# Kernel tuning notes

Measured on AMD Instinct MI355X. Metric: run time of the kernel, lower is better.

The kernel has to match this reference:

```python
import jax, jax.numpy as jnp
import numpy as np

N = 500000   # nodes per graph batch
E = 8000000  # edges per graph batch
B = 4096     # number of graphs
C = 2        # node feature dim
D = 2        # edge feature dim


def setup_inputs() -> dict:
    key = jax.random.key(0)
    ks = jax.random.split(key, 16)
    inp = {
        "x_a": jax.random.normal(ks[0], (N, C), jnp.float32),
        "edge_index_a": jax.random.randint(ks[1], (2, E), 0, N, jnp.int32),
        "edge_attr_a": jax.random.normal(ks[2], (E, D), jnp.float32),
        "batch_a": jnp.sort(jax.random.randint(ks[3], (N,), 0, B, jnp.int32)),
        "x_b": jax.random.normal(ks[4], (N, C), jnp.float32),
        "edge_index_b": jax.random.randint(ks[5], (2, E), 0, N, jnp.int32),
        "edge_attr_b": jax.random.normal(ks[6], (E, D), jnp.float32),
        "batch_b": jnp.sort(jax.random.randint(ks[7], (N,), 0, B, jnp.int32)),
        "targets": jax.random.normal(ks[8], (B,), jnp.float32),
        "num_graphs": B,
        # CGConv params: lin_f, lin_s each Linear(2*C+D=6 -> C)
        "Wf": jax.random.normal(ks[9], (2 * C + D, C), jnp.float32) * 0.4,
        "bf": jnp.zeros((C,), jnp.float32),
        "Ws": jax.random.normal(ks[10], (2 * C + D, C), jnp.float32) * 0.4,
        "bs": jnp.zeros((C,), jnp.float32),
        # l1: Linear(2 -> 3), l2: Linear(6 -> 1)
        "W1": jax.random.normal(ks[11], (C, 3), jnp.float32) * 0.5,
        "b1": jnp.zeros((3,), jnp.float32),
        "W2": jax.random.normal(ks[12], (6, 1), jnp.float32) * 0.4,
        "b2": jnp.zeros((1,), jnp.float32),
    }
    return inp


def cg_conv(x, edge_index, edge_attr, Wf, bf, Ws, bs):
    # PyG CGConv: out_i = x_i + sum_{j->i} sigmoid(lin_f(z)) * softplus(lin_s(z)),
    # z = [x_i, x_j, e_ij]; source_to_target flow => i = edge_index[1].
    src, dst = edge_index[0], edge_index[1]
    z = jnp.concatenate([x[dst], x[src], edge_attr], axis=1)  # [E, 6]
    m = jax.nn.sigmoid(z @ Wf + bf) * jax.nn.softplus(z @ Ws + bs)  # [E, C]
    agg = jax.ops.segment_sum(m, dst, num_segments=x.shape[0])
    return x + agg


def branch(x, edge_index, edge_attr, batch, num_graphs,
           Wf, bf, Ws, bs, W1, b1):
    h = cg_conv(x, edge_index, edge_attr, Wf, bf, Ws, bs)
    h = jax.nn.relu(h @ W1 + b1)  # [N, 3]
    sums = jax.ops.segment_sum(h, batch, num_segments=num_graphs)
    cnts = jax.ops.segment_sum(jnp.ones((h.shape[0],), h.dtype), batch,
                               num_segments=num_graphs)
    return sums / jnp.maximum(cnts, 1.0)[:, None]  # global_mean_pool [B, 3]


def reference(x_a, edge_index_a, edge_attr_a, batch_a,
              x_b, edge_index_b, edge_attr_b, batch_b,
              targets, num_graphs,
              Wf, bf, Ws, bs, W1, b1, W2, b2):
    out_1 = branch(x_a, edge_index_a, edge_attr_a, batch_a, num_graphs,
                   Wf, bf, Ws, bs, W1, b1)
    out_2 = branch(x_b, edge_index_b, edge_attr_b, batch_b, num_graphs,
                   Wf, bf, Ws, bs, W1, b1)
    out = jnp.concatenate([out_1, out_2], axis=1)  # [B, 6]
    out = jax.nn.relu(out @ W2 + b2)               # [B, 1]
    loss = jnp.mean((out[:, 0] - targets) ** 2)
    return out, loss
```

## Files before the change

kernel.cpp:

```cpp
#include <hip/hip_runtime.h>

#define N_NODES 500000
#define N_EDGES 8000000
#define N_GRAPHS 4096

#define NB 128
#define BIN_SHIFT 12
#define BIN_NODES 4096
#define NBINS 123
#define BIN_CAP 66560
#define T_EDGES 8192
#define P1_THREADS 512
#define EPT (T_EDGES / P1_THREADS)
#define P1_GRID ((N_EDGES + T_EDGES - 1) / T_EDGES)
#define K 4
#define P2_GRID (NBINS * K)
#define SLICE_F (BIN_NODES * 2)
#define FXS 131072.0f
#define FXI (1.0f / 131072.0f)
#define M_MAX 250.0f
#define OVF_CAP 8192

#define OFF_CURS_A   0
#define OFF_CURS_B   512
#define OFF_OVFC_A   1024
#define OFF_OVFC_B   1280
#define ZERO_SMALL   1536
#define OFF_STARTS_A 4096
#define OFF_STARTS_B 20736
#define OFF_MEAN_A   37376
#define OFF_MEAN_B   86528
#define OFF_OVF_A    135680
#define OFF_OVF_B    266752
#define OFF_SCRATCH  397824
#define OFF_BINS     16519680
#define WS_NEED      82014720ull

__global__ __launch_bounds__(512, 4) void p1_kernel(
    const float* __restrict__ x, const int* __restrict__ ei,
    const float* __restrict__ ea,
    const float* __restrict__ Wf, const float* __restrict__ bfv,
    const float* __restrict__ Ws, const float* __restrict__ bsv,
    unsigned long long* __restrict__ bins, unsigned int* __restrict__ cursors,
    unsigned int* __restrict__ ovf_cnt, float4* __restrict__ ovf)
{
    __shared__ unsigned long long sorted[T_EDGES];
    __shared__ unsigned int whist[8][NB];
    __shared__ unsigned int base[NB];
    __shared__ unsigned int cur[NB];
    __shared__ unsigned int gbase[NB];
    __shared__ unsigned int ntot_s;

    int t = threadIdx.x;
    int wave = t >> 6;
    int ebase = blockIdx.x * T_EDGES;

    for (int i = t; i < 8 * NB; i += P1_THREADS) ((unsigned int*)whist)[i] = 0;
    __syncthreads();

    int d[EPT];
#pragma unroll
    for (int i = 0; i < EPT; ++i) {
        int e = ebase + i * P1_THREADS + t;
        d[i] = (e < N_EDGES) ? ei[N_EDGES + e] : -1;
        if (d[i] >= 0)
            atomicAdd(&whist[wave][((unsigned)d[i]) >> BIN_SHIFT], 1u);
    }
    __syncthreads();

    if (t < 64) {
        unsigned tot0 = 0, tot1 = 0;
#pragma unroll
        for (int w = 0; w < 8; ++w) { tot0 += whist[w][2*t]; tot1 += whist[w][2*t+1]; }
        unsigned pair = tot0 + tot1;
        unsigned v = pair;
#pragma unroll
        for (int off = 1; off < 64; off <<= 1) {
            unsigned u = __shfl_up(v, off);
            if (t >= off) v += u;
        }
        unsigned excl = v - pair;
        base[2*t]   = excl;        cur[2*t]   = excl;
        base[2*t+1] = excl + tot0; cur[2*t+1] = excl + tot0;
        if (t == 63) ntot_s = v;
        gbase[2*t]   = tot0 ? atomicAdd(&cursors[2*t],   tot0) : 0u;
        gbase[2*t+1] = tot1 ? atomicAdd(&cursors[2*t+1], tot1) : 0u;
    }
    __syncthreads();

    float wf[12], wsv[12];
#pragma unroll
    for (int i = 0; i < 12; ++i) { wf[i] = Wf[i]; wsv[i] = Ws[i]; }
    float bf0 = bfv[0], bf1 = bfv[1], bs0 = bsv[0], bs1 = bsv[1];

#pragma unroll
    for (int i = 0; i < EPT; ++i) {
        int e = ebase + i * P1_THREADS + t;
        if (e >= N_EDGES) continue;
        int dst = d[i];
        int src = ei[e];
        float2 xd = ((const float2*)x)[dst];
        float2 xs = ((const float2*)x)[src];
        float2 ev = ((const float2*)ea)[e];
        float z0 = xd.x, z1 = xd.y, z2 = xs.x, z3 = xs.y, z4 = ev.x, z5 = ev.y;

        float f0 = bf0 + z0*wf[0] + z1*wf[2] + z2*wf[4] + z3*wf[6] + z4*wf[8]  + z5*wf[10];
        float f1 = bf1 + z0*wf[1] + z1*wf[3] + z2*wf[5] + z3*wf[7] + z4*wf[9]  + z5*wf[11];
        float s0 = bs0 + z0*wsv[0] + z1*wsv[2] + z2*wsv[4] + z3*wsv[6] + z4*wsv[8]  + z5*wsv[10];
        float s1 = bs1 + z0*wsv[1] + z1*wsv[3] + z2*wsv[5] + z3*wsv[7] + z4*wsv[9]  + z5*wsv[11];

        float m0 = (1.f/(1.f+__expf(-f0))) * (fmaxf(s0,0.f) + __logf(1.f+__expf(-fabsf(s0))));
        float m1 = (1.f/(1.f+__expf(-f1))) * (fmaxf(s1,0.f) + __logf(1.f+__expf(-fabsf(s1))));

        int b = (int)((unsigned)dst >> BIN_SHIFT);
        unsigned slot = atomicAdd(&cur[b], 1u);
        unsigned long long pk = 0ull;
        if (m0 < M_MAX && m1 < M_MAX) {
            unsigned fx0 = __float2uint_rn(m0 * FXS);
            unsigned fx1 = __float2uint_rn(m1 * FXS);
            pk = (unsigned long long)((unsigned)dst & (BIN_NODES - 1))
               | ((unsigned long long)fx0 << 12)
               | ((unsigned long long)fx1 << 37);
        } else {
            unsigned oi = atomicAdd(ovf_cnt, 1u);
            if (oi < OVF_CAP) ovf[oi] = make_float4(__int_as_float(dst), m0, m1, 0.f);
        }
        sorted[slot] = pk;
    }
    __syncthreads();

    int ntot = (int)ntot_s;
    for (int p = t; p < ntot; p += P1_THREADS) {
        int lo = 0, hi = NB - 1;
        while (lo < hi) {
            int mid = (lo + hi + 1) >> 1;
            if ((int)base[mid] <= p) lo = mid; else hi = mid - 1;
        }
        unsigned gpos = gbase[lo] + (unsigned)(p - (int)base[lo]);
        unsigned long long v = sorted[p];
        if (gpos < BIN_CAP) {
            bins[(size_t)lo * BIN_CAP + gpos] = v;
        } else {
            int local = (int)(v & (BIN_NODES - 1));
            float m0 = (float)((unsigned)((v >> 12) & 0x1FFFFFFu)) * FXI;
            float m1 = (float)((unsigned)((v >> 37) & 0x1FFFFFFu)) * FXI;
            int dst = (lo << BIN_SHIFT) + local;
            unsigned oi = atomicAdd(ovf_cnt, 1u);
            if (oi < OVF_CAP) ovf[oi] = make_float4(__int_as_float(dst), m0, m1, 0.f);
        }
    }
}

__global__ __launch_bounds__(512, 8) void p2_kernel(
    const unsigned long long* __restrict__ bins,
    const unsigned int* __restrict__ cursors,
    float* __restrict__ scratch)
{
    __shared__ float acc[SLICE_F];
    int b = blockIdx.x >> 2;
    int k = blockIdx.x & 3;
    int t = threadIdx.x;
#pragma unroll
    for (int i = t; i < SLICE_F; i += 512) acc[i] = 0.f;
    __syncthreads();

    int n = (int)min(cursors[b], (unsigned)BIN_CAP);
    int s = (n * k) / K, e = (n * (k + 1)) / K;
    const unsigned long long* bp = bins + (size_t)b * BIN_CAP;
    for (int i = s + t; i < e; i += 512) {
        unsigned long long v = bp[i];
        int local = (int)(v & (BIN_NODES - 1));
        float m0 = (float)((unsigned)((v >> 12) & 0x1FFFFFFu)) * FXI;
        float m1 = (float)((unsigned)((v >> 37) & 0x1FFFFFFu)) * FXI;
        atomicAdd(&acc[2 * local],     m0);
        atomicAdd(&acc[2 * local + 1], m1);
    }
    __syncthreads();

    float4* dst = (float4*)(scratch + (size_t)(b * K + k) * SLICE_F);
    const float4* src = (const float4*)acc;
#pragma unroll
    for (int i = t; i < SLICE_F / 4; i += 512) dst[i] = src[i];
}

__global__ __launch_bounds__(256) void ovf_kernel(
    const float4* __restrict__ ovf, const unsigned int* __restrict__ ovf_cnt,
    float* __restrict__ scratch)
{
    int n = (int)min(*ovf_cnt, (unsigned)OVF_CAP);
    for (int i = threadIdx.x; i < n; i += 256) {
        float4 r = ovf[i];
        int dst = __float_as_int(r.x);
        int b = dst >> BIN_SHIFT, local = dst & (BIN_NODES - 1);
        float* p = scratch + (size_t)(b * K) * SLICE_F + 2 * local;
        unsafeAtomicAdd(p,     r.y);
        unsafeAtomicAdd(p + 1, r.z);
    }
}

__global__ __launch_bounds__(256) void starts_kernel(
    const int* __restrict__ batch, unsigned int* __restrict__ starts)
{
    int i = blockIdx.x * 256 + threadIdx.x;
    if (i >= N_NODES) return;
    int b1 = batch[i];
    if (i == 0) {
        for (int g = 0; g <= b1; ++g) starts[g] = 0;
    } else {
        int b0 = batch[i - 1];
        for (int g = b0 + 1; g <= b1; ++g) starts[g] = i;
    }
    if (i == N_NODES - 1) {
        for (int g = b1 + 1; g <= N_GRAPHS; ++g) starts[g] = N_NODES;
    }
}

__global__ __launch_bounds__(256) void pool2_kernel(
    const float* __restrict__ x, const float* __restrict__ scratch,
    const unsigned int* __restrict__ starts,
    const float* __restrict__ W1, const float* __restrict__ b1,
    float* __restrict__ mean_out)
{
    int wave = threadIdx.x >> 6, lane = threadIdx.x & 63;
    int g = blockIdx.x * 4 + wave;

    float w00 = W1[0], w01 = W1[1], w02 = W1[2];
    float w10 = W1[3], w11 = W1[4], w12 = W1[5];
    float c0 = b1[0], c1 = b1[1], c2 = b1[2];

    const float2* sc2 = (const float2*)scratch;
    int s = (int)starts[g], e = (int)starts[g + 1];
    float a0 = 0.f, a1 = 0.f, a2 = 0.f;
    for (int i = s + lane; i < e; i += 64) {
        int b = i >> BIN_SHIFT, local = i & (BIN_NODES - 1);
        size_t f2base = (size_t)b * (K * BIN_NODES) + local;
        float2 g0 = sc2[f2base];
        float2 g1 = sc2[f2base + BIN_NODES];
        float2 g2 = sc2[f2base + 2 * BIN_NODES];
        float2 g3 = sc2[f2base + 3 * BIN_NODES];
        float2 xv = ((const float2*)x)[i];
        float h0 = xv.x + g0.x + g1.x + g2.x + g3.x;
        float h1 = xv.y + g0.y + g1.y + g2.y + g3.y;
        a0 += fmaxf(h0*w00 + h1*w10 + c0, 0.f);
        a1 += fmaxf(h0*w01 + h1*w11 + c1, 0.f);
        a2 += fmaxf(h0*w02 + h1*w12 + c2, 0.f);
    }
#pragma unroll
    for (int off = 32; off; off >>= 1) {
        a0 += __shfl_down(a0, off);
        a1 += __shfl_down(a1, off);
        a2 += __shfl_down(a2, off);
    }
    if (lane == 0) {
        float inv = 1.0f / fmaxf((float)(e - s), 1.0f);
        mean_out[3*(size_t)g]     = a0 * inv;
        mean_out[3*(size_t)g + 1] = a1 * inv;
        mean_out[3*(size_t)g + 2] = a2 * inv;
    }
}

__global__ __launch_bounds__(1024) void final_kernel(
    const float* __restrict__ ma, const float* __restrict__ mb,
    const float* __restrict__ W2, const float* __restrict__ b2,
    const float* __restrict__ targets,
    float* __restrict__ out)
{
    __shared__ float red[1024];
    float w0 = W2[0], w1 = W2[1], w2 = W2[2], w3 = W2[3], w4 = W2[4], w5 = W2[5];
    float bias = b2[0];

    float lsum = 0.f;
    for (int g = threadIdx.x; g < N_GRAPHS; g += 1024) {
        float v = bias
                + ma[3*(size_t)g]*w0 + ma[3*(size_t)g+1]*w1 + ma[3*(size_t)g+2]*w2
                + mb[3*(size_t)g]*w3 + mb[3*(size_t)g+1]*w4 + mb[3*(size_t)g+2]*w5;
        v = fmaxf(v, 0.f);
        out[g] = v;
        float d = v - targets[g];
        lsum += d * d;
    }
    red[threadIdx.x] = lsum;
    __syncthreads();
#pragma unroll
    for (int off = 512; off; off >>= 1) {
        if (threadIdx.x < (unsigned)off) red[threadIdx.x] += red[threadIdx.x + off];
        __syncthreads();
    }
    if (threadIdx.x == 0) out[N_GRAPHS] = red[0] * (1.0f / (float)N_GRAPHS);
}

#define FB_SCALE 4194304.0f
#define FB_INV   2.384185791015625e-07f

__global__ __launch_bounds__(256) void fb_edge_kernel(
    const float* __restrict__ x, const int* __restrict__ ei,
    const float* __restrict__ ea,
    const float* __restrict__ Wf, const float* __restrict__ bfv,
    const float* __restrict__ Ws, const float* __restrict__ bsv,
    unsigned long long* __restrict__ agg)
{
    float wf[12], ws[12];
#pragma unroll
    for (int i = 0; i < 12; ++i) { wf[i] = Wf[i]; ws[i] = Ws[i]; }
    float bf0 = bfv[0], bf1 = bfv[1], bs0 = bsv[0], bs1 = bsv[1];

    int e = blockIdx.x * 256 + threadIdx.x;
    int src = ei[e];
    int dst = ei[N_EDGES + e];
    float2 xd = ((const float2*)x)[dst];
    float2 xs = ((const float2*)x)[src];
    float2 ev = ((const float2*)ea)[e];
    float z0 = xd.x, z1 = xd.y, z2 = xs.x, z3 = xs.y, z4 = ev.x, z5 = ev.y;

    float f0 = bf0 + z0*wf[0] + z1*wf[2] + z2*wf[4] + z3*wf[6] + z4*wf[8]  + z5*wf[10];
    float f1 = bf1 + z0*wf[1] + z1*wf[3] + z2*wf[5] + z3*wf[7] + z4*wf[9]  + z5*wf[11];
    float s0 = bs0 + z0*ws[0] + z1*ws[2] + z2*ws[4] + z3*ws[6] + z4*ws[8]  + z5*ws[10];
    float s1 = bs1 + z0*ws[1] + z1*ws[3] + z2*ws[5] + z3*ws[7] + z4*ws[9]  + z5*ws[11];

    float m0 = (1.f/(1.f+__expf(-f0))) * (fmaxf(s0,0.f) + __logf(1.f+__expf(-fabsf(s0))));
    float m1 = (1.f/(1.f+__expf(-f1))) * (fmaxf(s1,0.f) + __logf(1.f+__expf(-fabsf(s1))));

    unsigned int fx0 = __float2uint_rn(m0 * FB_SCALE);
    unsigned int fx1 = __float2uint_rn(m1 * FB_SCALE);
    atomicAdd(&agg[dst], (unsigned long long)fx0 | ((unsigned long long)fx1 << 32));
}

__global__ __launch_bounds__(64) void fb_pool_kernel(
    const float* __restrict__ x, const unsigned long long* __restrict__ agg,
    const int* __restrict__ batch,
    const float* __restrict__ W1, const float* __restrict__ b1,
    float* __restrict__ mean_out)
{
    int b = blockIdx.x;
    float w00 = W1[0], w01 = W1[1], w02 = W1[2];
    float w10 = W1[3], w11 = W1[4], w12 = W1[5];
    float c0 = b1[0], c1 = b1[1], c2 = b1[2];

    int lo = 0, hi = N_NODES;
    while (lo < hi) { int mid = (lo + hi) >> 1; if (batch[mid] < b) lo = mid + 1; else hi = mid; }
    int seg_s = lo;
    hi = N_NODES;
    while (lo < hi) { int mid = (lo + hi) >> 1; if (batch[mid] < b + 1) lo = mid + 1; else hi = mid; }
    int seg_e = lo;

    float a0 = 0.f, a1 = 0.f, a2 = 0.f;
    for (int i = seg_s + (int)threadIdx.x; i < seg_e; i += 64) {
        unsigned long long v = agg[i];
        float g0 = (float)(unsigned int)(v & 0xffffffffull) * FB_INV;
        float g1 = (float)(unsigned int)(v >> 32) * FB_INV;
        float2 xv = ((const float2*)x)[i];
        float h0 = xv.x + g0, h1 = xv.y + g1;
        a0 += fmaxf(h0*w00 + h1*w10 + c0, 0.f);
        a1 += fmaxf(h0*w01 + h1*w11 + c1, 0.f);
        a2 += fmaxf(h0*w02 + h1*w12 + c2, 0.f);
    }
#pragma unroll
    for (int off = 32; off; off >>= 1) {
        a0 += __shfl_down(a0, off);
        a1 += __shfl_down(a1, off);
        a2 += __shfl_down(a2, off);
    }
    if (threadIdx.x == 0) {
        float inv = 1.0f / fmaxf((float)(seg_e - seg_s), 1.0f);
        mean_out[3*(size_t)b]     = a0 * inv;
        mean_out[3*(size_t)b + 1] = a1 * inv;
        mean_out[3*(size_t)b + 2] = a2 * inv;
    }
}

extern "C" void kernel_launch(void* const* d_in, const int* in_sizes, int n_in,
                              void* d_out, int out_size, void* d_ws, size_t ws_size,
                              hipStream_t stream) {
    const float* x_a     = (const float*)d_in[0];
    const int*   ei_a    = (const int*)  d_in[1];
    const float* ea_a    = (const float*)d_in[2];
    const int*   batch_a = (const int*)  d_in[3];
    const float* x_b     = (const float*)d_in[4];
    const int*   ei_b    = (const int*)  d_in[5];
    const float* ea_b    = (const float*)d_in[6];
    const int*   batch_b = (const int*)  d_in[7];
    const float* targets = (const float*)d_in[8];
    const float* Wf = (const float*)d_in[10];
    const float* bf = (const float*)d_in[11];
    const float* Ws = (const float*)d_in[12];
    const float* bs = (const float*)d_in[13];
    const float* W1 = (const float*)d_in[14];
    const float* b1 = (const float*)d_in[15];
    const float* W2 = (const float*)d_in[16];
    const float* b2 = (const float*)d_in[17];
    float* out = (float*)d_out;
    char* ws = (char*)d_ws;

    if (ws_size >= WS_NEED) {
        unsigned int* curs_a   = (unsigned int*)(ws + OFF_CURS_A);
        unsigned int* curs_b   = (unsigned int*)(ws + OFF_CURS_B);
        unsigned int* ovfc_a   = (unsigned int*)(ws + OFF_OVFC_A);
        unsigned int* ovfc_b   = (unsigned int*)(ws + OFF_OVFC_B);
        unsigned int* starts_a = (unsigned int*)(ws + OFF_STARTS_A);
        unsigned int* starts_b = (unsigned int*)(ws + OFF_STARTS_B);
        float* mean_a = (float*)(ws + OFF_MEAN_A);
        float* mean_b = (float*)(ws + OFF_MEAN_B);
        float4* ovf_a = (float4*)(ws + OFF_OVF_A);
        float4* ovf_b = (float4*)(ws + OFF_OVF_B);
        float* scratch = (float*)(ws + OFF_SCRATCH);
        unsigned long long* bins = (unsigned long long*)(ws + OFF_BINS);

        hipMemsetAsync(ws, 0, ZERO_SMALL, stream);

        int sgrid = (N_NODES + 255) / 256;
        starts_kernel<<<sgrid, 256, 0, stream>>>(batch_a, starts_a);
        starts_kernel<<<sgrid, 256, 0, stream>>>(batch_b, starts_b);

        p1_kernel<<<P1_GRID, P1_THREADS, 0, stream>>>(x_a, ei_a, ea_a, Wf, bf, Ws, bs,
                                                      bins, curs_a, ovfc_a, ovf_a);
        p2_kernel<<<P2_GRID, 512, 0, stream>>>(bins, curs_a, scratch);
        ovf_kernel<<<1, 256, 0, stream>>>(ovf_a, ovfc_a, scratch);
        pool2_kernel<<<N_GRAPHS / 4, 256, 0, stream>>>(x_a, scratch, starts_a, W1, b1, mean_a);

        p1_kernel<<<P1_GRID, P1_THREADS, 0, stream>>>(x_b, ei_b, ea_b, Wf, bf, Ws, bs,
                                                      bins, curs_b, ovfc_b, ovf_b);
        p2_kernel<<<P2_GRID, 512, 0, stream>>>(bins, curs_b, scratch);
        ovf_kernel<<<1, 256, 0, stream>>>(ovf_b, ovfc_b, scratch);
        pool2_kernel<<<N_GRAPHS / 4, 256, 0, stream>>>(x_b, scratch, starts_b, W1, b1, mean_b);

        final_kernel<<<1, 1024, 0, stream>>>(mean_a, mean_b, W2, b2, targets, out);
    } else {
        unsigned long long* aggu_a = (unsigned long long*)ws;
        unsigned long long* aggu_b = aggu_a + (size_t)N_NODES;
        float* mean_a = (float*)(aggu_b + (size_t)N_NODES);
        float* mean_b = mean_a + 3 * (size_t)N_GRAPHS;

        hipMemsetAsync(ws, 0, 2 * (size_t)N_NODES * sizeof(unsigned long long), stream);
        fb_edge_kernel<<<N_EDGES / 256, 256, 0, stream>>>(x_a, ei_a, ea_a, Wf, bf, Ws, bs, aggu_a);
        fb_edge_kernel<<<N_EDGES / 256, 256, 0, stream>>>(x_b, ei_b, ea_b, Wf, bf, Ws, bs, aggu_b);
        fb_pool_kernel<<<N_GRAPHS, 64, 0, stream>>>(x_a, aggu_a, batch_a, W1, b1, mean_a);
        fb_pool_kernel<<<N_GRAPHS, 64, 0, stream>>>(x_b, aggu_b, batch_b, W1, b1, mean_b);
        final_kernel<<<1, 1024, 0, stream>>>(mean_a, mean_b, W2, b2, targets, out);
    }
}
```

Measured before the change: 742.7 us.

## Shrink edge tiles, add nontemporal loads, replace bin search, split accumulator layout

```diff
diff --git a/kernel.cpp b/kernel.cpp
--- a/kernel.cpp
+++ b/kernel.cpp
@@ -9,7 +9,7 @@
 #define BIN_NODES 4096
 #define NBINS 123
 #define BIN_CAP 66560
-#define T_EDGES 8192
+#define T_EDGES 4096
 #define P1_THREADS 512
 #define EPT (T_EDGES / P1_THREADS)
 #define P1_GRID ((N_EDGES + T_EDGES - 1) / T_EDGES)
@@ -20,6 +20,7 @@
 #define FXI (1.0f / 131072.0f)
 #define M_MAX 250.0f
 #define OVF_CAP 8192
+#define SGRID ((N_NODES + 255) / 256)
 
 #define OFF_CURS_A   0
 #define OFF_CURS_B   512
@@ -36,7 +37,15 @@
 #define OFF_BINS     16519680
 #define WS_NEED      82014720ull
 
-__global__ __launch_bounds__(512, 4) void p1_kernel(
+__device__ __forceinline__ float2 ntload_f2(const float2* p) {
+    unsigned long long v = __builtin_nontemporal_load((const unsigned long long*)p);
+    float2 r;
+    r.x = __uint_as_float((unsigned int)v);
+    r.y = __uint_as_float((unsigned int)(v >> 32));
+    return r;
+}
+
+__global__ __launch_bounds__(512, 8) void p1_kernel(
     const float* __restrict__ x, const int* __restrict__ ei,
     const float* __restrict__ ea,
     const float* __restrict__ Wf, const float* __restrict__ bfv,
@@ -50,6 +59,7 @@
     __shared__ unsigned int cur[NB];
     __shared__ unsigned int gbase[NB];
     __shared__ unsigned int ntot_s;
+    unsigned char* binof = (unsigned char*)whist;
 
     int t = threadIdx.x;
     int wave = t >> 6;
@@ -62,12 +72,13 @@
 #pragma unroll
     for (int i = 0; i < EPT; ++i) {
         int e = ebase + i * P1_THREADS + t;
-        d[i] = (e < N_EDGES) ? ei[N_EDGES + e] : -1;
+        d[i] = (e < N_EDGES) ? __builtin_nontemporal_load(ei + N_EDGES + e) : -1;
         if (d[i] >= 0)
             atomicAdd(&whist[wave][((unsigned)d[i]) >> BIN_SHIFT], 1u);
     }
     __syncthreads();
 
+    unsigned g0 = 0, g1 = 0;
     if (t < 64) {
         unsigned tot0 = 0, tot1 = 0;
 #pragma unroll
@@ -83,8 +94,8 @@
         base[2*t]   = excl;        cur[2*t]   = excl;
         base[2*t+1] = excl + tot0; cur[2*t+1] = excl + tot0;
         if (t == 63) ntot_s = v;
-        gbase[2*t]   = tot0 ? atomicAdd(&cursors[2*t],   tot0) : 0u;
-        gbase[2*t+1] = tot1 ? atomicAdd(&cursors[2*t+1], tot1) : 0u;
+        g0 = tot0 ? atomicAdd(&cursors[2*t],   tot0) : 0u;
+        g1 = tot1 ? atomicAdd(&cursors[2*t+1], tot1) : 0u;
     }
     __syncthreads();
 
@@ -98,10 +109,10 @@
         int e = ebase + i * P1_THREADS + t;
         if (e >= N_EDGES) continue;
         int dst = d[i];
-        int src = ei[e];
+        int src = __builtin_nontemporal_load(ei + e);
         float2 xd = ((const float2*)x)[dst];
         float2 xs = ((const float2*)x)[src];
-        float2 ev = ((const float2*)ea)[e];
+        float2 ev = ntload_f2((const float2*)ea + e);
         float z0 = xd.x, z1 = xd.y, z2 = xs.x, z3 = xs.y, z4 = ev.x, z5 = ev.y;
 
         float f0 = bf0 + z0*wf[0] + z1*wf[2] + z2*wf[4] + z3*wf[6] + z4*wf[8]  + z5*wf[10];
@@ -126,20 +137,18 @@
             if (oi < OVF_CAP) ovf[oi] = make_float4(__int_as_float(dst), m0, m1, 0.f);
         }
         sorted[slot] = pk;
-    }
+        binof[slot] = (unsigned char)b;
+    }
+    if (t < 64) { gbase[2*t] = g0; gbase[2*t+1] = g1; }
     __syncthreads();
 
     int ntot = (int)ntot_s;
     for (int p = t; p < ntot; p += P1_THREADS) {
-        int lo = 0, hi = NB - 1;
-        while (lo < hi) {
-            int mid = (lo + hi + 1) >> 1;
-            if ((int)base[mid] <= p) lo = mid; else hi = mid - 1;
-        }
+        int lo = (int)binof[p];
         unsigned gpos = gbase[lo] + (unsigned)(p - (int)base[lo]);
         unsigned long long v = sorted[p];
         if (gpos < BIN_CAP) {
-            bins[(size_t)lo * BIN_CAP + gpos] = v;
+            __builtin_nontemporal_store(v, &bins[(size_t)lo * BIN_CAP + gpos]);
         } else {
             int local = (int)(v & (BIN_NODES - 1));
             float m0 = (float)((unsigned)((v >> 12) & 0x1FFFFFFu)) * FXI;
@@ -168,12 +177,12 @@
     int s = (n * k) / K, e = (n * (k + 1)) / K;
     const unsigned long long* bp = bins + (size_t)b * BIN_CAP;
     for (int i = s + t; i < e; i += 512) {
-        unsigned long long v = bp[i];
+        unsigned long long v = __builtin_nontemporal_load(bp + i);
         int local = (int)(v & (BIN_NODES - 1));
         float m0 = (float)((unsigned)((v >> 12) & 0x1FFFFFFu)) * FXI;
         float m1 = (float)((unsigned)((v >> 37) & 0x1FFFFFFu)) * FXI;
-        atomicAdd(&acc[2 * local],     m0);
-        atomicAdd(&acc[2 * local + 1], m1);
+        atomicAdd(&acc[local],             m0);
+        atomicAdd(&acc[BIN_NODES + local], m1);
     }
     __syncthreads();
 
@@ -192,16 +201,21 @@
         float4 r = ovf[i];
         int dst = __float_as_int(r.x);
         int b = dst >> BIN_SHIFT, local = dst & (BIN_NODES - 1);
-        float* p = scratch + (size_t)(b * K) * SLICE_F + 2 * local;
-        unsafeAtomicAdd(p,     r.y);
-        unsafeAtomicAdd(p + 1, r.z);
+        float* p = scratch + (size_t)(b * K) * SLICE_F;
+        unsafeAtomicAdd(p + local,             r.y);
+        unsafeAtomicAdd(p + BIN_NODES + local, r.z);
     }
 }
 
 __global__ __launch_bounds__(256) void starts_kernel(
-    const int* __restrict__ batch, unsigned int* __restrict__ starts)
-{
-    int i = blockIdx.x * 256 + threadIdx.x;
+    const int* __restrict__ ba, const int* __restrict__ bb,
+    unsigned int* __restrict__ sa, unsigned int* __restrict__ sb)
+{
+    int blk = blockIdx.x;
+    const int* batch = ba;
+    unsigned int* starts = sa;
+    if (blk >= SGRID) { blk -= SGRID; batch = bb; starts = sb; }
+    int i = blk * 256 + threadIdx.x;
     if (i >= N_NODES) return;
     int b1 = batch[i];
     if (i == 0) {
@@ -228,19 +242,17 @@
     float w10 = W1[3], w11 = W1[4], w12 = W1[5];
     float c0 = b1[0], c1 = b1[1], c2 = b1[2];
 
-    const float2* sc2 = (const float2*)scratch;
     int s = (int)starts[g], e = (int)starts[g + 1];
     float a0 = 0.f, a1 = 0.f, a2 = 0.f;
     for (int i = s + lane; i < e; i += 64) {
         int b = i >> BIN_SHIFT, local = i & (BIN_NODES - 1);
-        size_t f2base = (size_t)b * (K * BIN_NODES) + local;
-        float2 g0 = sc2[f2base];
-        float2 g1 = sc2[f2base + BIN_NODES];
-        float2 g2 = sc2[f2base + 2 * BIN_NODES];
-        float2 g3 = sc2[f2base + 3 * BIN_NODES];
+        const float* sl = scratch + (size_t)(b * K) * SLICE_F + local;
+        float h0 = sl[0] + sl[SLICE_F] + sl[2*SLICE_F] + sl[3*SLICE_F];
+        float h1 = sl[BIN_NODES] + sl[BIN_NODES + SLICE_F]
+                 + sl[BIN_NODES + 2*SLICE_F] + sl[BIN_NODES + 3*SLICE_F];
         float2 xv = ((const float2*)x)[i];
-        float h0 = xv.x + g0.x + g1.x + g2.x + g3.x;
-        float h1 = xv.y + g0.y + g1.y + g2.y + g3.y;
+        h0 += xv.x;
+        h1 += xv.y;
         a0 += fmaxf(h0*w00 + h1*w10 + c0, 0.f);
         a1 += fmaxf(h0*w01 + h1*w11 + c1, 0.f);
         a2 += fmaxf(h0*w02 + h1*w12 + c2, 0.f);
@@ -407,9 +419,7 @@
 
         hipMemsetAsync(ws, 0, ZERO_SMALL, stream);
 
-        int sgrid = (N_NODES + 255) / 256;
-        starts_kernel<<<sgrid, 256, 0, stream>>>(batch_a, starts_a);
-        starts_kernel<<<sgrid, 256, 0, stream>>>(batch_b, starts_b);
+        starts_kernel<<<2 * SGRID, 256, 0, stream>>>(batch_a, batch_b, starts_a, starts_b);
 
         p1_kernel<<<P1_GRID, P1_THREADS, 0, stream>>>(x_a, ei_a, ea_a, Wf, bf, Ws, bs,
                                                       bins, curs_a, ovfc_a, ovf_a);
```

Result: faster. 717.7 us (-3.4%).
